# Kernel tuning notes

Measured on AMD Instinct MI355X. Metric: run time of the kernel, lower is better.

## Reference

```python
import jax, jax.numpy as jnp
import numpy as np

D = 512
B, S1, S2 = 8, 2048, 2048


def setup_inputs() -> dict:
    key = jax.random.key(0)
    ks = jax.random.split(key, 8)
    s = 1.0 / np.sqrt(D)
    return {
        "x1": jax.random.normal(ks[0], (B, S1, D), dtype=jnp.float32),
        "x2": jax.random.normal(ks[1], (B, S2, D), dtype=jnp.float32),
        "Wq": jax.random.normal(ks[2], (D, D), dtype=jnp.float32) * s,
        "bq": jnp.zeros((D,), dtype=jnp.float32),
        "Wk": jax.random.normal(ks[3], (D, D), dtype=jnp.float32) * s,
        "bk": jnp.zeros((D,), dtype=jnp.float32),
        "Wv": jax.random.normal(ks[4], (D, D), dtype=jnp.float32) * s,
        "bv": jnp.zeros((D,), dtype=jnp.float32),
    }


def reference(x1, x2, Wq, bq, Wk, bk, Wv, bv):
    # q,k,v projections (torch Linear: x @ W^T + b)
    q = jnp.einsum("bsd,ed->bse", x1, Wq) + bq  # [B,S1,D]
    k = jnp.einsum("btd,ed->bte", x2, Wk) + bk  # [B,S2,D]
    v = jnp.einsum("btd,ed->bte", x2, Wv) + bv  # [B,S2,D]
    # NOTE: source scales by input_dim (D), not sqrt(D)
    scores = jnp.einsum("bse,bte->bst", q, k) / D  # [B,S1,S2]
    attn = jax.nn.softmax(scores, axis=-1)
    return jnp.einsum("bst,bte->bse", attn, v)  # [B,S1,D]
```

## Files before the change

kernel.cpp:

```cpp
#include <hip/hip_runtime.h>

using u8  = unsigned char;
using u16 = unsigned short;
using u32 = unsigned int;
using s16x8 = __attribute__((ext_vector_type(8))) short;
using bf16x8 = __attribute__((ext_vector_type(8))) __bf16;
using f32x4 = __attribute__((ext_vector_type(4))) float;
using i32x4 = __attribute__((ext_vector_type(4))) int;
using i32x8 = __attribute__((ext_vector_type(8))) int;

__device__ inline u16 f2bf(float f) {
  u32 u = __float_as_uint(f);
  u = (u + 0x7FFFu + ((u >> 16) & 1u)) >> 16;
  return (u16)u;
}

__device__ inline u8 f2fp8(float f) {
  return (u8)(__builtin_amdgcn_cvt_pk_fp8_f32(f, f, 0, false) & 0xFF);
}

__device__ inline f32x4 mfma16(s16x8 a, s16x8 b, f32x4 c) {
  return __builtin_amdgcn_mfma_f32_16x16x32_bf16(
      __builtin_bit_cast(bf16x8, a), __builtin_bit_cast(bf16x8, b), c, 0, 0, 0);
}

__device__ inline f32x4 mfma_fp8(i32x8 a, i32x8 b, f32x4 c) {
  return __builtin_amdgcn_mfma_scale_f32_16x16x128_f8f6f4(
      a, b, c, 0 , 0 , 0, 127, 0, 127);
}

__device__ inline void load_lds16(const void* g, void* l) {
  __builtin_amdgcn_global_load_lds(
      (const __attribute__((address_space(1))) void*)g,
      (__attribute__((address_space(3))) void*)l, 16, 0, 0);
}

__device__ inline s16x8 cvt8(f32x4 lo, f32x4 hi) {
  u32 w0, w1, w2, w3;
  asm("v_cvt_pk_bf16_f32 %0, %1, %2" : "=v"(w0) : "v"(lo[0]), "v"(lo[1]));
  asm("v_cvt_pk_bf16_f32 %0, %1, %2" : "=v"(w1) : "v"(lo[2]), "v"(lo[3]));
  asm("v_cvt_pk_bf16_f32 %0, %1, %2" : "=v"(w2) : "v"(hi[0]), "v"(hi[1]));
  asm("v_cvt_pk_bf16_f32 %0, %1, %2" : "=v"(w3) : "v"(hi[2]), "v"(hi[3]));
  i32x4 r;
  r[0] = (int)w0; r[1] = (int)w1; r[2] = (int)w2; r[3] = (int)w3;
  return __builtin_bit_cast(s16x8, r);
}

__global__ __launch_bounds__(256) void cast_w3z(
    const float* __restrict__ a, const float* __restrict__ b,
    const float* __restrict__ c, u16* __restrict__ oa, u16* __restrict__ ob,
    u16* __restrict__ oc) {
  const float* in = blockIdx.y == 0 ? a : (blockIdx.y == 1 ? b : c);
  u16* out = blockIdx.y == 0 ? oa : (blockIdx.y == 1 ? ob : oc);
  int i = (blockIdx.x * 256 + threadIdx.x) * 4;
  float4 f = *(const float4*)(in + i);
  ushort4 o;
  o.x = f2bf(f.x); o.y = f2bf(f.y); o.z = f2bf(f.z); o.w = f2bf(f.w);
  *(ushort4*)(out + i) = o;
}

__global__ __launch_bounds__(256) void gemm_qkv(
    const float* __restrict__ x1, const float* __restrict__ x2,
    const u16* __restrict__ Wq, const u16* __restrict__ Wk,
    const u16* __restrict__ Wv, u8* __restrict__ qb8, u8* __restrict__ kb8,
    u16* __restrict__ vTb, const float* __restrict__ bq,
    const float* __restrict__ bk, const float* __restrict__ bv) {
  int flat = blockIdx.x + 12 * blockIdx.y;
  flat = (flat & 7) * 192 + (flat >> 3);
  const int col = flat % 12;
  const int m0 = (flat / 12) * 128;

  const float* Ax; const u16* Bw; const float* bias; int n0w, mode;
  if (col < 4)      { Ax = x1; Bw = Wq; bias = bq; n0w = col * 128;       mode = 0; }
  else if (col < 8) { Ax = x2; Bw = Wk; bias = bk; n0w = (col - 4) * 128; mode = 1; }
  else              { Ax = x2; Bw = Wv; bias = bv; n0w = (col - 8) * 128; mode = 2; }

  const int tid = threadIdx.x;
  const int lane = tid & 63;
  const int wave = tid >> 6;
  const int wm = (wave >> 1) * 64;
  const int wn = (wave & 1) * 64;

  __shared__ float Asf[128 * 64];
  __shared__ u16 Bs[128 * 64];

  const int sr = lane >> 3;
  const int gd = (lane & 7) ^ sr;
  const int fr = lane & 15;
  const int fg = lane >> 4;

  f32x4 acc[4][4];
#pragma unroll
  for (int i = 0; i < 4; ++i)
#pragma unroll
    for (int j = 0; j < 4; ++j) acc[i][j] = 0.0f;

  for (int k0 = 0; k0 < 512; k0 += 64) {
#pragma unroll
    for (int it = 0; it < 8; ++it) {
      const int idx = wave * 8 + it;
      const int row = idx * 4 + (lane >> 4);
      const int gs = (lane & 15) ^ (row & 15);
      load_lds16(Ax + (size_t)(m0 + row) * 512 + k0 + gs * 4, &Asf[idx * 256]);
    }
#pragma unroll
    for (int it = 0; it < 4; ++it) {
      const int ch = wave * 4 + it;
      const int rowb = ch * 8 + sr;
      load_lds16(Bw + (size_t)(n0w + rowb) * 512 + k0 + gd * 8, &Bs[ch * 512]);
    }
    __syncthreads();
#pragma unroll
    for (int s = 0; s < 2; ++s) {
      s16x8 af[4], bfr[4];
#pragma unroll
      for (int i = 0; i < 4; ++i) {
        const int rowa = wm + i * 16 + fr;
        const float* Ar = &Asf[rowa * 64];
        const int g0 = 2 * (s * 4 + fg);
        f32x4 lo = *(const f32x4*)&Ar[(g0 ^ fr) * 4];
        f32x4 hi = *(const f32x4*)&Ar[((g0 + 1) ^ fr) * 4];
        af[i] = cvt8(lo, hi);
        const int slot = ((s * 4 + fg) ^ (fr & 7)) * 8;
        bfr[i] = *(const s16x8*)&Bs[(wn + i * 16 + fr) * 64 + slot];
      }
#pragma unroll
      for (int mi = 0; mi < 4; ++mi)
#pragma unroll
        for (int ni = 0; ni < 4; ++ni)
          acc[mi][ni] = mfma16(af[mi], bfr[ni], acc[mi][ni]);
    }
    __syncthreads();
  }

  const int er = fg * 4;
  const int ec = fr;

  if (mode != 2) {
    u8* Cb = (mode == 0) ? qb8 : kb8;
#pragma unroll
    for (int mi = 0; mi < 4; ++mi)
#pragma unroll
      for (int ni = 0; ni < 4; ++ni) {
        const int colg = n0w + wn + ni * 16 + ec;
        const float badd = bias[colg];
#pragma unroll
        for (int i = 0; i < 4; ++i) {
          const int row = m0 + wm + mi * 16 + er + i;
          Cb[(size_t)row * 512 + colg] = f2fp8(acc[mi][ni][i] + badd);
        }
      }
  } else {
    u16* Tb = (u16*)Asf;
    const int batch = m0 >> 11;
    const int srow = m0 & 2047;
    u16* Cv = vTb + (size_t)batch * (512 * 2048);
#pragma unroll
    for (int h = 0; h < 2; ++h) {
      if ((wn >> 6) == h) {
#pragma unroll
        for (int mi = 0; mi < 4; ++mi)
#pragma unroll
          for (int ni = 0; ni < 4; ++ni) {
            const int c = ni * 16 + ec;
            const float badd = bias[n0w + wn + c];
#pragma unroll
            for (int i = 0; i < 4; ++i) {
              const int r = wm + mi * 16 + er + i;
              Tb[c * 136 + r] = f2bf(acc[mi][ni][i] + badd);
            }
          }
      }
      __syncthreads();
      const int d = tid >> 2;
      const int sc = (tid & 3) * 32;
      const int dglob = n0w + 64 * h + d;
#pragma unroll
      for (int j = 0; j < 4; ++j) {
        uint4 v = *(const uint4*)&Tb[d * 136 + sc + j * 8];
        *(uint4*)&Cv[(size_t)dglob * 2048 + srow + sc + j * 8] = v;
      }
      __syncthreads();
    }
  }
}

__global__ __launch_bounds__(512, 2) void attn_fused(
    const u8* __restrict__ q8, const u8* __restrict__ k8,
    const u16* __restrict__ vT, float* __restrict__ out) {
  const int batch = blockIdx.x;
  const int q0 = blockIdx.y * 64;
  const u8* qb = q8 + ((size_t)batch * 2048 + q0) * 512;
  const u8* kb = k8 + (size_t)batch * 2048 * 512;
  const u16* vb = vT + (size_t)batch * 512 * 2048;
  float* ob = out + ((size_t)batch * 2048 + q0) * 512;

  const int tid = threadIdx.x;
  const int lane = tid & 63;
  const int wave = tid >> 6;
  const int wm = (wave >> 1) * 16;
  const int wn = (wave & 1) * 32;
  const int wd = wave * 64;
  const int sr = lane >> 3;
  const int gd = (lane & 7) ^ sr;
  const int fr = lane & 15;
  const int fg = lane >> 4;
  const int r7 = fr & 7;
  const int s0 = (2 * fg) ^ r7;
  const int s1 = s0 ^ 1;

  __shared__ u8 Ks[2][4][8192];
  __shared__ u16 Ps[2][64 * 64];

  i32x8 Qf[4];
#pragma unroll
  for (int kc = 0; kc < 4; ++kc) {
    const u8* p = qb + (size_t)(wm + fr) * 512 + kc * 128 + fg * 32;
    i32x4 lo = *(const i32x4*)p;
    i32x4 hi = *(const i32x4*)(p + 16);
    i32x8 q;
    q[0] = lo[0]; q[1] = lo[1]; q[2] = lo[2]; q[3] = lo[3];
    q[4] = hi[0]; q[5] = hi[1]; q[6] = hi[2]; q[7] = hi[3];
    Qf[kc] = q;
  }

  auto stageK = [&](int kv0, int buf) {
#pragma unroll
    for (int it = 0; it < 4; ++it) {
      const int idx = wave * 4 + it;
      const int kc = idx >> 3, sub = idx & 7;
      load_lds16(kb + (size_t)(kv0 + sub * 8 + sr) * 512 + kc * 128 + gd * 16,
                 &Ks[buf][kc][sub * 1024]);
    }
  };
  s16x8 Vr[8];
  auto loadV = [&](int kv0) {
#pragma unroll
    for (int ks = 0; ks < 2; ++ks)
#pragma unroll
      for (int ni = 0; ni < 4; ++ni)
        Vr[ks * 4 + ni] = *(const s16x8*)&vb[(size_t)(wd + ni * 16 + fr) * 2048 +
                                             kv0 + ks * 32 + fg * 8];
  };

  f32x4 oacc[4][4];
#pragma unroll
  for (int i = 0; i < 4; ++i)
#pragma unroll
    for (int j = 0; j < 4; ++j) oacc[i][j] = 0.0f;
  float l_reg[4] = {0.0f, 0.0f, 0.0f, 0.0f};

  constexpr int NT = 32;

  auto tile = [&](int t, int psel) {
    f32x4 sacc[2];
    sacc[0] = 0.0f; sacc[1] = 0.0f;
#pragma unroll
    for (int kc = 0; kc < 4; ++kc) {
#pragma unroll
      for (int ni = 0; ni < 2; ++ni) {
        const u8* pb = &Ks[psel][kc][(wn + ni * 16 + fr) * 128];
        i32x4 blo = *(const i32x4*)(pb + s0 * 16);
        i32x4 bhi = *(const i32x4*)(pb + s1 * 16);
        i32x8 bK;
        bK[0] = blo[0]; bK[1] = blo[1]; bK[2] = blo[2]; bK[3] = blo[3];
        bK[4] = bhi[0]; bK[5] = bhi[1]; bK[6] = bhi[2]; bK[7] = bhi[3];
        __builtin_amdgcn_s_setprio(1);
        sacc[ni] = mfma_fp8(Qf[kc], bK, sacc[ni]);
        __builtin_amdgcn_s_setprio(0);
      }
    }
    u16* Pd = &Ps[psel][0];
#pragma unroll
    for (int ni = 0; ni < 2; ++ni) {
      const int g = (wn >> 3) + ni * 2 + (fr >> 3);
      const int co = fr & 7;
#pragma unroll
      for (int i = 0; i < 4; ++i) {
        const int r = wm + fg * 4 + i;
        const int ph = ((r >> 2) & 1) * 4 + ((r ^ (r >> 3)) & 1) * 2 +
                       ((r >> 1) & 1);
        const float p = __expf(sacc[ni][i] * (1.0f / 512.0f));
        l_reg[i] += p;
        Pd[r * 64 + ((g ^ ph) << 3) + co] = f2bf(p);
      }
    }
    __syncthreads();
    if (t + 2 < NT) stageK((t + 2) * 64, psel);
#pragma unroll
    for (int ks = 0; ks < 2; ++ks) {
      s16x8 pa[4];
#pragma unroll
      for (int mi = 0; mi < 4; ++mi) {
        const int r = mi * 16 + fr;
        const int ph = ((r >> 2) & 1) * 4 + ((r ^ (r >> 3)) & 1) * 2 +
                       ((r >> 1) & 1);
        pa[mi] = *(const s16x8*)&Pd[r * 64 + (((ks * 4 + fg) ^ ph) << 3)];
      }
      __builtin_amdgcn_s_setprio(1);
#pragma unroll
      for (int ni = 0; ni < 4; ++ni)
#pragma unroll
        for (int mi = 0; mi < 4; ++mi)
          oacc[mi][ni] = mfma16(pa[mi], Vr[ks * 4 + ni], oacc[mi][ni]);
      __builtin_amdgcn_s_setprio(0);
    }
    if (t + 1 < NT) loadV((t + 1) * 64);
  };

  stageK(0, 0);
  loadV(0);
  __syncthreads();
  stageK(64, 1);

  for (int tt = 0; tt < NT; tt += 2) {
    tile(tt, 0);
    tile(tt + 1, 1);
  }

  float* lsc = (float*)&Ps[0][0];
  __syncthreads();
#pragma unroll
  for (int i = 0; i < 4; ++i) {
    float rs = l_reg[i];
    rs += __shfl_xor(rs, 1);
    rs += __shfl_xor(rs, 2);
    rs += __shfl_xor(rs, 4);
    rs += __shfl_xor(rs, 8);
    if (fr == 0) lsc[(wn >> 5) * 64 + wm + fg * 4 + i] = rs;
  }
  __syncthreads();

#pragma unroll
  for (int mi = 0; mi < 4; ++mi)
#pragma unroll
    for (int i = 0; i < 4; ++i) {
      const int r = mi * 16 + fg * 4 + i;
      const float l = lsc[r] + lsc[64 + r];
      const float li = __builtin_amdgcn_rcpf(l);
#pragma unroll
      for (int ni = 0; ni < 4; ++ni)
        ob[(size_t)r * 512 + wd + ni * 16 + fr] = oacc[mi][ni][i] * li;
    }
}

extern "C" void kernel_launch(void* const* d_in, const int* in_sizes, int n_in,
                              void* d_out, int out_size, void* d_ws, size_t ws_size,
                              hipStream_t stream) {
  constexpr int B = 8, S = 2048, D = 512;
  constexpr size_t MS = (size_t)B * S;

  const float* x1 = (const float*)d_in[0];
  const float* x2 = (const float*)d_in[1];
  const float* Wq = (const float*)d_in[2];
  const float* bq = (const float*)d_in[3];
  const float* Wk = (const float*)d_in[4];
  const float* bk = (const float*)d_in[5];
  const float* Wv = (const float*)d_in[6];
  const float* bv = (const float*)d_in[7];
  float* out = (float*)d_out;

  u16* x1b = (u16*)d_ws;
  u16* x2b = x1b + MS * D;
  u16* Wqb = x2b + MS * D;
  u16* Wkb = Wqb + (size_t)D * D;
  u16* Wvb = Wkb + (size_t)D * D;
  u16* vTb = Wvb + (size_t)D * D;
  u16* Sc  = vTb + MS * D;
  float* lbuf = (float*)(Sc + (size_t)B * S * S);
  u8* qb8 = (u8*)(lbuf + MS);
  u8* kb8 = qb8 + MS * D;

  dim3 blk(256);

  cast_w3z<<<dim3((D * D) / 1024, 3), blk, 0, stream>>>(
      Wq, Wk, Wv, Wqb, Wkb, Wvb);

  gemm_qkv<<<dim3(12, 128), blk, 0, stream>>>(
      x1, x2, Wqb, Wkb, Wvb, qb8, kb8, vTb, bq, bk, bv);

  attn_fused<<<dim3(8, 32, 1), dim3(512), 0, stream>>>(qb8, kb8, vTb, out);
}
```

Measured before the change: 259.6 us.

## Pre-cast activations to bf16 and double-buffer the projection GEMM

```diff
diff --git a/kernel.cpp b/kernel.cpp
--- a/kernel.cpp
+++ b/kernel.cpp
@@ -35,34 +35,36 @@
       (__attribute__((address_space(3))) void*)l, 16, 0, 0);
 }
 
-__device__ inline s16x8 cvt8(f32x4 lo, f32x4 hi) {
-  u32 w0, w1, w2, w3;
-  asm("v_cvt_pk_bf16_f32 %0, %1, %2" : "=v"(w0) : "v"(lo[0]), "v"(lo[1]));
-  asm("v_cvt_pk_bf16_f32 %0, %1, %2" : "=v"(w1) : "v"(lo[2]), "v"(lo[3]));
-  asm("v_cvt_pk_bf16_f32 %0, %1, %2" : "=v"(w2) : "v"(hi[0]), "v"(hi[1]));
-  asm("v_cvt_pk_bf16_f32 %0, %1, %2" : "=v"(w3) : "v"(hi[2]), "v"(hi[3]));
-  i32x4 r;
-  r[0] = (int)w0; r[1] = (int)w1; r[2] = (int)w2; r[3] = (int)w3;
-  return __builtin_bit_cast(s16x8, r);
-}
-
-__global__ __launch_bounds__(256) void cast_w3z(
-    const float* __restrict__ a, const float* __restrict__ b,
-    const float* __restrict__ c, u16* __restrict__ oa, u16* __restrict__ ob,
-    u16* __restrict__ oc) {
-  const float* in = blockIdx.y == 0 ? a : (blockIdx.y == 1 ? b : c);
-  u16* out = blockIdx.y == 0 ? oa : (blockIdx.y == 1 ? ob : oc);
-  int i = (blockIdx.x * 256 + threadIdx.x) * 4;
+__global__ __launch_bounds__(256) void cast_all(
+    const float* __restrict__ x1, const float* __restrict__ x2,
+    const float* __restrict__ wq, const float* __restrict__ wk,
+    const float* __restrict__ wv, u16* __restrict__ o1, u16* __restrict__ o2,
+    u16* __restrict__ oq, u16* __restrict__ ok, u16* __restrict__ ov) {
+  const float* in;
+  u16* out;
+  int bx = blockIdx.x;
+  if (blockIdx.y == 0) {
+    in = x1; out = o1;
+  } else if (blockIdx.y == 1) {
+    in = x2; out = o2;
+  } else {
+    if (bx >= 768) return;
+    const int w = bx >> 8;
+    in = w == 0 ? wq : (w == 1 ? wk : wv);
+    out = w == 0 ? oq : (w == 1 ? ok : ov);
+    bx &= 255;
+  }
+  int i = (bx * 256 + threadIdx.x) * 4;
   float4 f = *(const float4*)(in + i);
   ushort4 o;
   o.x = f2bf(f.x); o.y = f2bf(f.y); o.z = f2bf(f.z); o.w = f2bf(f.w);
   *(ushort4*)(out + i) = o;
 }
 
-__global__ __launch_bounds__(256) void gemm_qkv(
-    const float* __restrict__ x1, const float* __restrict__ x2,
-    const u16* __restrict__ Wq, const u16* __restrict__ Wk,
-    const u16* __restrict__ Wv, u8* __restrict__ qb8, u8* __restrict__ kb8,
+__global__ __launch_bounds__(256) void gemm_proj(
+    const u16* __restrict__ x1b, const u16* __restrict__ x2b,
+    const u16* __restrict__ Wqb, const u16* __restrict__ Wkb,
+    const u16* __restrict__ Wvb, u8* __restrict__ qb8, u8* __restrict__ kb8,
     u16* __restrict__ vTb, const float* __restrict__ bq,
     const float* __restrict__ bk, const float* __restrict__ bv) {
   int flat = blockIdx.x + 12 * blockIdx.y;
@@ -70,10 +72,10 @@
   const int col = flat % 12;
   const int m0 = (flat / 12) * 128;
 
-  const float* Ax; const u16* Bw; const float* bias; int n0w, mode;
-  if (col < 4)      { Ax = x1; Bw = Wq; bias = bq; n0w = col * 128;       mode = 0; }
-  else if (col < 8) { Ax = x2; Bw = Wk; bias = bk; n0w = (col - 4) * 128; mode = 1; }
-  else              { Ax = x2; Bw = Wv; bias = bv; n0w = (col - 8) * 128; mode = 2; }
+  const u16* Ax; const u16* Bw; const float* bias; int n0w, mode;
+  if (col < 4)      { Ax = x1b; Bw = Wqb; bias = bq; n0w = col * 128;       mode = 0; }
+  else if (col < 8) { Ax = x2b; Bw = Wkb; bias = bk; n0w = (col - 4) * 128; mode = 1; }
+  else              { Ax = x2b; Bw = Wvb; bias = bv; n0w = (col - 8) * 128; mode = 2; }
 
   const int tid = threadIdx.x;
   const int lane = tid & 63;
@@ -81,54 +83,52 @@
   const int wm = (wave >> 1) * 64;
   const int wn = (wave & 1) * 64;
 
-  __shared__ float Asf[128 * 64];
-  __shared__ u16 Bs[128 * 64];
+  __shared__ u16 As_[2][128 * 64];
+  __shared__ u16 Bs_[2][128 * 64];
 
   const int sr = lane >> 3;
   const int gd = (lane & 7) ^ sr;
   const int fr = lane & 15;
   const int fg = lane >> 4;
 
-  f32x4 acc[4][4];
-#pragma unroll
-  for (int i = 0; i < 4; ++i)
-#pragma unroll
-    for (int j = 0; j < 4; ++j) acc[i][j] = 0.0f;
-
-  for (int k0 = 0; k0 < 512; k0 += 64) {
-#pragma unroll
-    for (int it = 0; it < 8; ++it) {
-      const int idx = wave * 8 + it;
-      const int row = idx * 4 + (lane >> 4);
-      const int gs = (lane & 15) ^ (row & 15);
-      load_lds16(Ax + (size_t)(m0 + row) * 512 + k0 + gs * 4, &Asf[idx * 256]);
-    }
+  auto stage = [&](int k0, int b) {
 #pragma unroll
     for (int it = 0; it < 4; ++it) {
       const int ch = wave * 4 + it;
-      const int rowb = ch * 8 + sr;
-      load_lds16(Bw + (size_t)(n0w + rowb) * 512 + k0 + gd * 8, &Bs[ch * 512]);
-    }
-    __syncthreads();
+      const int row = ch * 8 + sr;
+      load_lds16(Ax + (size_t)(m0 + row) * 512 + k0 + gd * 8, &As_[b][ch * 512]);
+      load_lds16(Bw + (size_t)(n0w + row) * 512 + k0 + gd * 8, &Bs_[b][ch * 512]);
+    }
+  };
+
+  f32x4 acc[4][4];
+#pragma unroll
+  for (int i = 0; i < 4; ++i)
+#pragma unroll
+    for (int j = 0; j < 4; ++j) acc[i][j] = 0.0f;
+
+  stage(0, 0);
+  __syncthreads();
+
+  for (int ks = 0; ks < 8; ++ks) {
+    const int b = ks & 1;
+    if (ks < 7) stage((ks + 1) * 64, b ^ 1);
 #pragma unroll
     for (int s = 0; s < 2; ++s) {
+      const int slot = ((s * 4 + fg) ^ (fr & 7)) * 8;
       s16x8 af[4], bfr[4];
 #pragma unroll
       for (int i = 0; i < 4; ++i) {
-        const int rowa = wm + i * 16 + fr;
-        const float* Ar = &Asf[rowa * 64];
-        const int g0 = 2 * (s * 4 + fg);
-        f32x4 lo = *(const f32x4*)&Ar[(g0 ^ fr) * 4];
-        f32x4 hi = *(const f32x4*)&Ar[((g0 + 1) ^ fr) * 4];
-        af[i] = cvt8(lo, hi);
-        const int slot = ((s * 4 + fg) ^ (fr & 7)) * 8;
-        bfr[i] = *(const s16x8*)&Bs[(wn + i * 16 + fr) * 64 + slot];
-      }
+        af[i]  = *(const s16x8*)&As_[b][(wm + i * 16 + fr) * 64 + slot];
+        bfr[i] = *(const s16x8*)&Bs_[b][(wn + i * 16 + fr) * 64 + slot];
+      }
+      __builtin_amdgcn_s_setprio(1);
 #pragma unroll
       for (int mi = 0; mi < 4; ++mi)
 #pragma unroll
         for (int ni = 0; ni < 4; ++ni)
           acc[mi][ni] = mfma16(af[mi], bfr[ni], acc[mi][ni]);
+      __builtin_amdgcn_s_setprio(0);
     }
     __syncthreads();
   }
@@ -151,7 +151,7 @@
         }
       }
   } else {
-    u16* Tb = (u16*)Asf;
+    u16* Tb = &As_[0][0];
     const int batch = m0 >> 11;
     const int srow = m0 & 2047;
     u16* Cv = vTb + (size_t)batch * (512 * 2048);
@@ -255,6 +255,7 @@
   auto tile = [&](int t, int psel) {
     f32x4 sacc[2];
     sacc[0] = 0.0f; sacc[1] = 0.0f;
+    __builtin_amdgcn_s_setprio(1);
 #pragma unroll
     for (int kc = 0; kc < 4; ++kc) {
 #pragma unroll
@@ -265,11 +266,10 @@
         i32x8 bK;
         bK[0] = blo[0]; bK[1] = blo[1]; bK[2] = blo[2]; bK[3] = blo[3];
         bK[4] = bhi[0]; bK[5] = bhi[1]; bK[6] = bhi[2]; bK[7] = bhi[3];
-        __builtin_amdgcn_s_setprio(1);
         sacc[ni] = mfma_fp8(Qf[kc], bK, sacc[ni]);
-        __builtin_amdgcn_s_setprio(0);
-      }
-    }
+      }
+    }
+    __builtin_amdgcn_s_setprio(0);
     u16* Pd = &Ps[psel][0];
 #pragma unroll
     for (int ni = 0; ni < 2; ++ni) {
@@ -373,11 +373,11 @@
 
   dim3 blk(256);
 
-  cast_w3z<<<dim3((D * D) / 1024, 3), blk, 0, stream>>>(
-      Wq, Wk, Wv, Wqb, Wkb, Wvb);
-
-  gemm_qkv<<<dim3(12, 128), blk, 0, stream>>>(
-      x1, x2, Wqb, Wkb, Wvb, qb8, kb8, vTb, bq, bk, bv);
+  cast_all<<<dim3((MS * D) / 1024, 3), blk, 0, stream>>>(
+      x1, x2, Wq, Wk, Wv, x1b, x2b, Wqb, Wkb, Wvb);
+
+  gemm_proj<<<dim3(12, 128), blk, 0, stream>>>(
+      x1b, x2b, Wqb, Wkb, Wvb, qb8, kb8, vTb, bq, bk, bv);
 
   attn_fused<<<dim3(8, 32, 1), dim3(512), 0, stream>>>(qb8, kb8, vTb, out);
 }
```

After: 253.8 us. 2.2% less time.
